# Kernel tuning notes

Hardware: AMD Instinct MI355X
Metric: run time of the kernel (lower is better)

The kernel has to match this reference:

```python
import jax, jax.numpy as jnp
import numpy as np

N = 50000   # nodes
E = 600000  # edges
F = 128     # num_node_features
H = 128     # hidden_channels
C = 10      # num_classes
G = 64      # graphs in batch


def setup_inputs() -> dict:
    key = jax.random.key(0)
    ks = jax.random.split(key, 12)
    x = jax.random.normal(ks[0], (N, F), jnp.float32)
    edge_index = jax.random.randint(ks[1], (2, E), 0, N, dtype=jnp.int32)
    batch = jnp.sort(jax.random.randint(ks[2], (N,), 0, G, dtype=jnp.int32))
    def glorot(k, shape):
        lim = np.sqrt(6.0 / (shape[0] + shape[1])).astype(np.float32)
        return jax.random.uniform(k, shape, jnp.float32, -lim, lim)
    return {
        "x": x,
        "edge_index": edge_index,
        "batch": batch,
        "W1": glorot(ks[3], (F, H)), "b1": jnp.zeros((H,), jnp.float32),
        "W2": glorot(ks[4], (H, H)), "b2": jnp.zeros((H,), jnp.float32),
        "W3": glorot(ks[5], (H, H)), "b3": jnp.zeros((H,), jnp.float32),
        "Wl": glorot(ks[6], (H, C)), "bl": jnp.zeros((C,), jnp.float32),
    }


def reference(x, edge_index, batch, W1, b1, W2, b2, W3, b3, Wl, bl):
    # GCNConv: add self-loops, symmetric degree normalization D^-1/2 A D^-1/2
    src0, dst0 = edge_index[0], edge_index[1]
    loop = jnp.arange(N, dtype=src0.dtype)
    src = jnp.concatenate([src0, loop])
    dst = jnp.concatenate([dst0, loop])
    deg = jax.ops.segment_sum(jnp.ones_like(dst, jnp.float32), dst, num_segments=N)
    dinv = jnp.where(deg > 0, jax.lax.rsqrt(deg), 0.0)
    norm = dinv[src] * dinv[dst]  # [E+N]

    def conv(h, W, b):
        h = h @ W                                  # [N, H] transform first (PyG GCNConv)
        msg = h[src] * norm[:, None]               # gather + normalize
        return jax.ops.segment_sum(msg, dst, num_segments=N) + b  # scatter-add

    h = jax.nn.relu(conv(x, W1, b1))
    h = jax.nn.relu(conv(h, W2, b2))
    h = conv(h, W3, b3)

    # global_mean_pool over batch ids
    counts = jax.ops.segment_sum(jnp.ones((N,), jnp.float32), batch, num_segments=G)
    pooled = jax.ops.segment_sum(h, batch, num_segments=G) / jnp.maximum(counts, 1.0)[:, None]
    return pooled @ Wl + bl  # [G, C]
```

## Files before the change

### kernel.cpp

```cpp
#include <hip/hip_runtime.h>
#include <hip/hip_bf16.h>

#define NN 50000
#define EE 600000
#define FF 128
#define HH 128
#define CC 10
#define GG 64

typedef unsigned int uint32;
typedef unsigned short ushort16;
typedef __attribute__((ext_vector_type(8))) short short8;
typedef __attribute__((ext_vector_type(4))) float f32x4;

__device__ __forceinline__ float bf_lo(uint32 u) { return __uint_as_float(u << 16); }
__device__ __forceinline__ float bf_hi(uint32 u) { return __uint_as_float(u & 0xffff0000u); }
__device__ __forceinline__ ushort16 f2bf(float f) {
    __hip_bfloat16 b = __float2bfloat16(f);
    return *reinterpret_cast<ushort16*>(&b);
}
__device__ __forceinline__ uint32 pack2bf(float a, float b) {
    return (uint32)f2bf(a) | ((uint32)f2bf(b) << 16);
}
__device__ __forceinline__ int q8(float f) {
    return __float2int_rn(fminf(fmaxf(f * 16.f, -127.f), 127.f)) & 255;
}

__global__ void count_deg(const int* __restrict__ dst, int* __restrict__ deg) {
    int e = blockIdx.x * blockDim.x + threadIdx.x;
    if (e < EE) atomicAdd(&deg[dst[e]], 1);
}

__global__ void compute_dinv(const int* __restrict__ deg, float* __restrict__ dinv) {
    int n = blockIdx.x * blockDim.x + threadIdx.x;
    if (n < NN) dinv[n] = rsqrtf((float)(deg[n] + 1));
}

#define SB 256
__global__ __launch_bounds__(SB) void scan_block(const int* __restrict__ deg,
                                                 int* __restrict__ row_ptr,
                                                 int* __restrict__ bsum) {
    __shared__ int sm[SB];
    int t = threadIdx.x;
    int i = blockIdx.x * SB + t;
    int v = (i < NN) ? deg[i] : 0;
    sm[t] = v;
    __syncthreads();
    for (int off = 1; off < SB; off <<= 1) {
        int add = (t >= off) ? sm[t - off] : 0;
        __syncthreads();
        sm[t] += add;
        __syncthreads();
    }
    if (i < NN) row_ptr[i] = sm[t] - v;
    if (t == SB - 1) bsum[blockIdx.x] = sm[t];
}

__global__ void scan_bsum(int* __restrict__ bsum, int nb) {
    __shared__ int sm[256];
    int t = threadIdx.x;
    int v = (t < nb) ? bsum[t] : 0;
    sm[t] = v;
    __syncthreads();
    for (int off = 1; off < 256; off <<= 1) {
        int add = (t >= off) ? sm[t - off] : 0;
        __syncthreads();
        sm[t] += add;
        __syncthreads();
    }
    if (t < nb) bsum[t] = sm[t] - v;
}

__global__ __launch_bounds__(SB) void scan_add(int* __restrict__ row_ptr,
                                               const int* __restrict__ bsum) {
    int i = blockIdx.x * SB + threadIdx.x;
    if (i < NN) row_ptr[i] += bsum[blockIdx.x];
    if (i == 0) row_ptr[NN] = EE;
}

__global__ void fill_csr(const int* __restrict__ src, const int* __restrict__ dst,
                         const int* __restrict__ row_ptr, int* __restrict__ cursor,
                         const float* __restrict__ dinv,
                         int2* __restrict__ csr_en) {
    int e = blockIdx.x * blockDim.x + threadIdx.x;
    if (e < EE) {
        int s = src[e], d = dst[e];
        int pos = row_ptr[d] + atomicAdd(&cursor[d], 1);
        csr_en[pos] = make_int2(s * 128, __float_as_int(dinv[s] * dinv[d] * 0.0625f));
    }
}

__global__ __launch_bounds__(256) void transpose_w3(const float* __restrict__ W1,
                                                    const float* __restrict__ W2,
                                                    const float* __restrict__ W3,
                                                    ushort16* __restrict__ T1,
                                                    ushort16* __restrict__ T2,
                                                    ushort16* __restrict__ T3) {
    int wi = blockIdx.x >> 4;
    const float* W = (wi == 0) ? W1 : (wi == 1) ? W2 : W3;
    ushort16* T = (wi == 0) ? T1 : (wi == 1) ? T2 : T3;
    int base = (blockIdx.x & 15) * 256 + threadIdx.x;
#pragma unroll
    for (int i = 0; i < 4; i++) {
        int idx = base + i * 4096;
        int col = idx & 127;
        int k = idx >> 7;
        T[col * 128 + k] = f2bf(W[k * 128 + col]);
    }
}

template <bool AF32>
__global__ __launch_bounds__(256) void gemm_mfma(const void* __restrict__ Av,
                                                 const ushort16* __restrict__ Wt,
                                                 uint32* __restrict__ zout) {
    __shared__ uint4 lds4[34816 / 16];
    char* lds = (char*)lds4;
    int t = threadIdx.x;
    int w = t >> 6, l = t & 63;
    int lrow = l & 15, g = l >> 4;
    int rowBase = blockIdx.x * 64;
    int arow = rowBase + w * 16 + lrow;
    short8 afr[4];
    const char* Ab = (const char*)Av;
    bool inb = arow < NN;
#pragma unroll
    for (int s = 0; s < 4; s++) {
        if (inb) {
            if (AF32) {
                float4 f0 = *(const float4*)(Ab + (size_t)arow * 512 + s * 128 + g * 32);
                float4 f1 = *(const float4*)(Ab + (size_t)arow * 512 + s * 128 + g * 32 + 16);
                union { short8 s8; uint32 u[4]; } cv;
                cv.u[0] = pack2bf(f0.x, f0.y);
                cv.u[1] = pack2bf(f0.z, f0.w);
                cv.u[2] = pack2bf(f1.x, f1.y);
                cv.u[3] = pack2bf(f1.z, f1.w);
                afr[s] = cv.s8;
            } else {
                afr[s] = *(const short8*)(Ab + (size_t)arow * 256 + s * 64 + g * 16);
            }
        } else {
            short8 z = {0, 0, 0, 0, 0, 0, 0, 0};
            afr[s] = z;
        }
    }
    const char* Wb = (const char*)Wt;
#pragma unroll
    for (int i = 0; i < 8; i++) {
        int idx = t + i * 256;
        int col = idx >> 4, c16 = idx & 15;
        *(uint4*)(lds + col * 272 + c16 * 16) = *(const uint4*)(Wb + col * 256 + c16 * 16);
    }
    __syncthreads();
    f32x4 acc[8];
#pragma unroll
    for (int c = 0; c < 8; c++) { f32x4 z = {0.f, 0.f, 0.f, 0.f}; acc[c] = z; }
#pragma unroll
    for (int s = 0; s < 4; s++) {
#pragma unroll
        for (int c = 0; c < 8; c++) {
            short8 b = *(const short8*)(lds + (c * 16 + lrow) * 272 + s * 64 + g * 16);
            acc[c] = __builtin_amdgcn_mfma_f32_16x16x32_bf16(afr[s], b, acc[c], 0, 0, 0);
        }
    }
    __syncthreads();
    char* myl = lds + w * 8448;
#pragma unroll
    for (int c = 0; c < 8; c++) {
#pragma unroll
        for (int j = 0; j < 4; j++) {
            *(float*)(myl + (g * 4 + j) * 528 + (c * 16 + lrow) * 4) = acc[c][j];
        }
    }
    __syncthreads();
#pragma unroll
    for (int j = 0; j < 8; j++) {
        int rl = (l >> 5) + 2 * j;
        int ch = l & 31;
        float4 v = *(const float4*)(myl + rl * 528 + ch * 16);
        int grow = rowBase + w * 16 + rl;
        if (grow < NN) {
            uint32 u = q8(v.x) | (q8(v.y) << 8) | (q8(v.z) << 16) | (q8(v.w) << 24);
            zout[(size_t)grow * 32 + ch] = u;
        }
    }
}

#define AGG_FMA(c, v)                                              \
    {                                                              \
        float nm = __int_as_float((c).y);                          \
        a0 += nm * (float)((int)((v) << 24) >> 24);                \
        a1 += nm * (float)((int)((v) << 16) >> 24);                \
        a2 += nm * (float)((int)((v) << 8) >> 24);                 \
        a3 += nm * (float)((int)(v) >> 24);                        \
    }

template <int MODE>
__global__ __launch_bounds__(256) void aggregate(const uint32* __restrict__ z8,
                                                 const int* __restrict__ row_ptr,
                                                 const int2* __restrict__ csr_en,
                                                 const float* __restrict__ dinv,
                                                 const float* __restrict__ bias,
                                                 ushort16* __restrict__ out,
                                                 float* __restrict__ pooled,
                                                 const int* __restrict__ batch) {
    int grp = threadIdx.x >> 5;
    int ll  = threadIdx.x & 31;
    int n = blockIdx.x * 8 + grp;
    const char* base = (const char*)z8;
    int boff = ll << 2;
    float dn = dinv[n];
    float w2 = dn * dn * 0.0625f;
    float a0, a1, a2, a3;
    {
        uint32 u = *(const uint32*)(base + (size_t)n * 128 + boff);
        a0 = w2 * (float)((int)(u << 24) >> 24);
        a1 = w2 * (float)((int)(u << 16) >> 24);
        a2 = w2 * (float)((int)(u << 8) >> 24);
        a3 = w2 * (float)((int)u >> 24);
    }
    int s = row_ptr[n], e = row_ptr[n + 1];
    int k = s;
    if (k + 4 <= e) {
        int2 c0 = csr_en[k], c1 = csr_en[k + 1], c2 = csr_en[k + 2], c3 = csr_en[k + 3];
        uint32 v0 = *(const uint32*)(base + (size_t)(uint32)c0.x + boff);
        uint32 v1 = *(const uint32*)(base + (size_t)(uint32)c1.x + boff);
        uint32 v2 = *(const uint32*)(base + (size_t)(uint32)c2.x + boff);
        uint32 v3 = *(const uint32*)(base + (size_t)(uint32)c3.x + boff);
        k += 4;
        for (; k + 4 <= e; k += 4) {
            int2 d0 = csr_en[k], d1 = csr_en[k + 1], d2 = csr_en[k + 2], d3 = csr_en[k + 3];
            uint32 w0 = *(const uint32*)(base + (size_t)(uint32)d0.x + boff);
            uint32 w1 = *(const uint32*)(base + (size_t)(uint32)d1.x + boff);
            uint32 w2_ = *(const uint32*)(base + (size_t)(uint32)d2.x + boff);
            uint32 w3 = *(const uint32*)(base + (size_t)(uint32)d3.x + boff);
            AGG_FMA(c0, v0); AGG_FMA(c1, v1); AGG_FMA(c2, v2); AGG_FMA(c3, v3);
            c0 = d0; c1 = d1; c2 = d2; c3 = d3;
            v0 = w0; v1 = w1; v2 = w2_; v3 = w3;
        }
        AGG_FMA(c0, v0); AGG_FMA(c1, v1); AGG_FMA(c2, v2); AGG_FMA(c3, v3);
    }
    for (; k < e; k++) {
        int2 c0 = csr_en[k];
        uint32 v0 = *(const uint32*)(base + (size_t)(uint32)c0.x + boff);
        AGG_FMA(c0, v0);
    }
    float4 b4 = *(const float4*)(bias + (ll << 2));
    a0 += b4.x; a1 += b4.y; a2 += b4.z; a3 += b4.w;
    if (MODE == 0) {
        a0 = fmaxf(a0, 0.f); a1 = fmaxf(a1, 0.f); a2 = fmaxf(a2, 0.f); a3 = fmaxf(a3, 0.f);
        uint2 o = make_uint2(pack2bf(a0, a1), pack2bf(a2, a3));
        *(uint2*)((char*)out + (size_t)n * 256 + (ll << 3)) = o;
    }
    if (MODE == 2) {
        __shared__ float psum[2][128];
        __shared__ int sgmin;
        int g = batch[n];
        if (threadIdx.x == 0) sgmin = g;
        psum[threadIdx.x >> 7][threadIdx.x & 127] = 0.f;
        __syncthreads();
        int slot = g - sgmin;
        if (slot < 2) {
            float* p = &psum[slot][ll << 2];
            atomicAdd(p + 0, a0); atomicAdd(p + 1, a1);
            atomicAdd(p + 2, a2); atomicAdd(p + 3, a3);
        } else {
            float* p = &pooled[g * HH + (ll << 2)];
            atomicAdd(p + 0, a0); atomicAdd(p + 1, a1);
            atomicAdd(p + 2, a2); atomicAdd(p + 3, a3);
        }
        __syncthreads();
        int sl = threadIdx.x >> 7, f = threadIdx.x & 127;
        float v = psum[sl][f];
        int gg = sgmin + sl;
        if (v != 0.f && gg < GG) atomicAdd(&pooled[gg * HH + f], v);
    }
}

__global__ __launch_bounds__(128) void final_linear(const float* __restrict__ pooled,
                                                    const int* __restrict__ batch,
                                                    const float* __restrict__ Wl,
                                                    const float* __restrict__ bl,
                                                    float* __restrict__ out) {
    int g = blockIdx.x;
    int t = threadIdx.x;
    __shared__ float pm[128];
    __shared__ int cnt_s;
    if (t == 0) {
        int lo = 0, hi = NN;
        while (lo < hi) { int m = (lo + hi) >> 1; if (batch[m] < g) lo = m + 1; else hi = m; }
        int s = lo;
        lo = 0; hi = NN;
        while (lo < hi) { int m = (lo + hi) >> 1; if (batch[m] < g + 1) lo = m + 1; else hi = m; }
        int c = lo - s;
        cnt_s = c > 0 ? c : 1;
    }
    __syncthreads();
    pm[t] = pooled[g * HH + t] / (float)cnt_s;
    __syncthreads();
    if (t < CC) {
        float o = bl[t];
        for (int f = 0; f < 128; f++) o += pm[f] * Wl[f * CC + t];
        out[g * CC + t] = o;
    }
}

extern "C" void kernel_launch(void* const* d_in, const int* in_sizes, int n_in,
                              void* d_out, int out_size, void* d_ws, size_t ws_size,
                              hipStream_t stream) {
    const float* x    = (const float*)d_in[0];
    const int*   ei   = (const int*)d_in[1];
    const int*   bat  = (const int*)d_in[2];
    const float* W1   = (const float*)d_in[3];
    const float* b1   = (const float*)d_in[4];
    const float* W2   = (const float*)d_in[5];
    const float* b2   = (const float*)d_in[6];
    const float* W3   = (const float*)d_in[7];
    const float* b3   = (const float*)d_in[8];
    const float* Wl   = (const float*)d_in[9];
    const float* bl   = (const float*)d_in[10];
    float* out = (float*)d_out;

    const int* src = ei;
    const int* dst = ei + EE;

    char* ws = (char*)d_ws;
    size_t off = 0;
    auto take = [&](size_t bytes) -> char* {
        char* p = ws + off;
        off += (bytes + 255) & ~(size_t)255;
        return p;
    };
    int*      deg     = (int*)take((size_t)NN * 4);
    float*    dinv    = (float*)take((size_t)NN * 4);
    int*      row_ptr = (int*)take((size_t)(NN + 1) * 4);
    int*      bsum    = (int*)take((size_t)256 * 4);
    int2*     csr_en  = (int2*)take((size_t)EE * 8);
    ushort16* Wt1     = (ushort16*)take((size_t)HH * HH * 2);
    ushort16* Wt2     = (ushort16*)take((size_t)HH * HH * 2);
    ushort16* Wt3     = (ushort16*)take((size_t)HH * HH * 2);
    uint32*   bufZ    = (uint32*)take((size_t)NN * HH);
    ushort16* bufH    = (ushort16*)take((size_t)NN * HH * 2);
    float*    pooled  = (float*)take((size_t)GG * HH * 4);

    const int nbScan = (NN + SB - 1) / SB;

    hipMemsetAsync(deg, 0, (size_t)NN * 4, stream);
    hipMemsetAsync(pooled, 0, (size_t)GG * HH * 4, stream);
    count_deg<<<(EE + 255) / 256, 256, 0, stream>>>(dst, deg);
    compute_dinv<<<(NN + 255) / 256, 256, 0, stream>>>(deg, dinv);
    scan_block<<<nbScan, SB, 0, stream>>>(deg, row_ptr, bsum);
    scan_bsum<<<1, 256, 0, stream>>>(bsum, nbScan);
    scan_add<<<nbScan, SB, 0, stream>>>(row_ptr, bsum);
    hipMemsetAsync(deg, 0, (size_t)NN * 4, stream);
    fill_csr<<<(EE + 255) / 256, 256, 0, stream>>>(src, dst, row_ptr, deg, dinv, csr_en);

    transpose_w3<<<48, 256, 0, stream>>>(W1, W2, W3, Wt1, Wt2, Wt3);

    const int gemmBlocks = (NN + 63) / 64;
    const int aggBlocks  = NN / 8;
    gemm_mfma<true><<<gemmBlocks, 256, 0, stream>>>(x, Wt1, bufZ);
    aggregate<0><<<aggBlocks, 256, 0, stream>>>(bufZ, row_ptr, csr_en, dinv, b1, bufH, pooled, bat);
    gemm_mfma<false><<<gemmBlocks, 256, 0, stream>>>(bufH, Wt2, bufZ);
    aggregate<0><<<aggBlocks, 256, 0, stream>>>(bufZ, row_ptr, csr_en, dinv, b2, bufH, pooled, bat);
    gemm_mfma<false><<<gemmBlocks, 256, 0, stream>>>(bufH, Wt3, bufZ);
    aggregate<2><<<aggBlocks, 256, 0, stream>>>(bufZ, row_ptr, csr_en, dinv, b3, bufH, pooled, bat);

    final_linear<<<GG, 128, 0, stream>>>(pooled, bat, Wl, bl, out);
}
```

Measured before the change: 212.0 us.

## Split int8 feature table into two column halves and aggregate each half separately

The GEMM output is now written as two 64-byte-per-row int8 tables (low and high feature halves), and each aggregation layer runs as two passes, one per half, with 16 threads per node. Each pass gathers from a table half the size (about 3.2 MB), which is meant to raise the L2/cache hit rate of the random neighbor gathers. In exchange, CSR indices, row pointers and norms are read twice per layer, there are twice as many aggregate launches, and the pooled atomics and LDS partial sums are split across passes.

```diff
diff --git a/kernel.cpp b/kernel.cpp
--- a/kernel.cpp
+++ b/kernel.cpp
@@ -86,7 +86,7 @@
     if (e < EE) {
         int s = src[e], d = dst[e];
         int pos = row_ptr[d] + atomicAdd(&cursor[d], 1);
-        csr_en[pos] = make_int2(s * 128, __float_as_int(dinv[s] * dinv[d] * 0.0625f));
+        csr_en[pos] = make_int2(s * 64, __float_as_int(dinv[s] * dinv[d] * 0.0625f));
     }
 }
 
@@ -112,7 +112,8 @@
 template <bool AF32>
 __global__ __launch_bounds__(256) void gemm_mfma(const void* __restrict__ Av,
                                                  const ushort16* __restrict__ Wt,
-                                                 uint32* __restrict__ zout) {
+                                                 uint32* __restrict__ zlo,
+                                                 uint32* __restrict__ zhi) {
     __shared__ uint4 lds4[34816 / 16];
     char* lds = (char*)lds4;
     int t = threadIdx.x;
@@ -180,7 +181,8 @@
         int grow = rowBase + w * 16 + rl;
         if (grow < NN) {
             uint32 u = q8(v.x) | (q8(v.y) << 8) | (q8(v.z) << 16) | (q8(v.w) << 24);
-            zout[(size_t)grow * 32 + ch] = u;
+            if (ch < 16) zlo[(size_t)grow * 16 + ch] = u;
+            else         zhi[(size_t)grow * 16 + (ch - 16)] = u;
         }
     }
 }
@@ -195,24 +197,25 @@
     }
 
 template <int MODE>
-__global__ __launch_bounds__(256) void aggregate(const uint32* __restrict__ z8,
+__global__ __launch_bounds__(256) void aggregate(const uint32* __restrict__ zp,
                                                  const int* __restrict__ row_ptr,
                                                  const int2* __restrict__ csr_en,
                                                  const float* __restrict__ dinv,
                                                  const float* __restrict__ bias,
                                                  ushort16* __restrict__ out,
                                                  float* __restrict__ pooled,
-                                                 const int* __restrict__ batch) {
-    int grp = threadIdx.x >> 5;
-    int ll  = threadIdx.x & 31;
-    int n = blockIdx.x * 8 + grp;
-    const char* base = (const char*)z8;
+                                                 const int* __restrict__ batch,
+                                                 int pass) {
+    int grp = threadIdx.x >> 4;
+    int ll  = threadIdx.x & 15;
+    int n = blockIdx.x * 16 + grp;
+    const char* base = (const char*)zp;
     int boff = ll << 2;
     float dn = dinv[n];
     float w2 = dn * dn * 0.0625f;
     float a0, a1, a2, a3;
     {
-        uint32 u = *(const uint32*)(base + (size_t)n * 128 + boff);
+        uint32 u = *(const uint32*)(base + (size_t)n * 64 + boff);
         a0 = w2 * (float)((int)(u << 24) >> 24);
         a1 = w2 * (float)((int)(u << 16) >> 24);
         a2 = w2 * (float)((int)(u << 8) >> 24);
@@ -244,19 +247,19 @@
         uint32 v0 = *(const uint32*)(base + (size_t)(uint32)c0.x + boff);
         AGG_FMA(c0, v0);
     }
-    float4 b4 = *(const float4*)(bias + (ll << 2));
+    float4 b4 = *(const float4*)(bias + pass * 64 + (ll << 2));
     a0 += b4.x; a1 += b4.y; a2 += b4.z; a3 += b4.w;
     if (MODE == 0) {
         a0 = fmaxf(a0, 0.f); a1 = fmaxf(a1, 0.f); a2 = fmaxf(a2, 0.f); a3 = fmaxf(a3, 0.f);
         uint2 o = make_uint2(pack2bf(a0, a1), pack2bf(a2, a3));
-        *(uint2*)((char*)out + (size_t)n * 256 + (ll << 3)) = o;
+        *(uint2*)((char*)out + (size_t)n * 256 + pass * 128 + (ll << 3)) = o;
     }
     if (MODE == 2) {
-        __shared__ float psum[2][128];
+        __shared__ float psum[2][64];
         __shared__ int sgmin;
         int g = batch[n];
         if (threadIdx.x == 0) sgmin = g;
-        psum[threadIdx.x >> 7][threadIdx.x & 127] = 0.f;
+        if (threadIdx.x < 128) psum[threadIdx.x >> 6][threadIdx.x & 63] = 0.f;
         __syncthreads();
         int slot = g - sgmin;
         if (slot < 2) {
@@ -264,15 +267,17 @@
             atomicAdd(p + 0, a0); atomicAdd(p + 1, a1);
             atomicAdd(p + 2, a2); atomicAdd(p + 3, a3);
         } else {
-            float* p = &pooled[g * HH + (ll << 2)];
+            float* p = &pooled[g * HH + pass * 64 + (ll << 2)];
             atomicAdd(p + 0, a0); atomicAdd(p + 1, a1);
             atomicAdd(p + 2, a2); atomicAdd(p + 3, a3);
         }
         __syncthreads();
-        int sl = threadIdx.x >> 7, f = threadIdx.x & 127;
-        float v = psum[sl][f];
-        int gg = sgmin + sl;
-        if (v != 0.f && gg < GG) atomicAdd(&pooled[gg * HH + f], v);
+        if (threadIdx.x < 128) {
+            int sl = threadIdx.x >> 6, f = threadIdx.x & 63;
+            float v = psum[sl][f];
+            int gg = sgmin + sl;
+            if (v != 0.f && gg < GG) atomicAdd(&pooled[gg * HH + pass * 64 + f], v);
+        }
     }
 }
 
@@ -338,7 +343,8 @@
     ushort16* Wt1     = (ushort16*)take((size_t)HH * HH * 2);
     ushort16* Wt2     = (ushort16*)take((size_t)HH * HH * 2);
     ushort16* Wt3     = (ushort16*)take((size_t)HH * HH * 2);
-    uint32*   bufZ    = (uint32*)take((size_t)NN * HH);
+    uint32*   zlo     = (uint32*)take((size_t)NN * 64);
+    uint32*   zhi     = (uint32*)take((size_t)NN * 64);
     ushort16* bufH    = (ushort16*)take((size_t)NN * HH * 2);
     float*    pooled  = (float*)take((size_t)GG * HH * 4);
 
@@ -357,13 +363,16 @@
     transpose_w3<<<48, 256, 0, stream>>>(W1, W2, W3, Wt1, Wt2, Wt3);
 
     const int gemmBlocks = (NN + 63) / 64;
-    const int aggBlocks  = NN / 8;
-    gemm_mfma<true><<<gemmBlocks, 256, 0, stream>>>(x, Wt1, bufZ);
-    aggregate<0><<<aggBlocks, 256, 0, stream>>>(bufZ, row_ptr, csr_en, dinv, b1, bufH, pooled, bat);
-    gemm_mfma<false><<<gemmBlocks, 256, 0, stream>>>(bufH, Wt2, bufZ);
-    aggregate<0><<<aggBlocks, 256, 0, stream>>>(bufZ, row_ptr, csr_en, dinv, b2, bufH, pooled, bat);
-    gemm_mfma<false><<<gemmBlocks, 256, 0, stream>>>(bufH, Wt3, bufZ);
-    aggregate<2><<<aggBlocks, 256, 0, stream>>>(bufZ, row_ptr, csr_en, dinv, b3, bufH, pooled, bat);
+    const int aggBlocks  = NN / 16;
+    gemm_mfma<true><<<gemmBlocks, 256, 0, stream>>>(x, Wt1, zlo, zhi);
+    aggregate<0><<<aggBlocks, 256, 0, stream>>>(zlo, row_ptr, csr_en, dinv, b1, bufH, pooled, bat, 0);
+    aggregate<0><<<aggBlocks, 256, 0, stream>>>(zhi, row_ptr, csr_en, dinv, b1, bufH, pooled, bat, 1);
+    gemm_mfma<false><<<gemmBlocks, 256, 0, stream>>>(bufH, Wt2, zlo, zhi);
+    aggregate<0><<<aggBlocks, 256, 0, stream>>>(zlo, row_ptr, csr_en, dinv, b2, bufH, pooled, bat, 0);
+    aggregate<0><<<aggBlocks, 256, 0, stream>>>(zhi, row_ptr, csr_en, dinv, b2, bufH, pooled, bat, 1);
+    gemm_mfma<false><<<gemmBlocks, 256, 0, stream>>>(bufH, Wt3, zlo, zhi);
+    aggregate<2><<<aggBlocks, 256, 0, stream>>>(zlo, row_ptr, csr_en, dinv, b3, bufH, pooled, bat, 0);
+    aggregate<2><<<aggBlocks, 256, 0, stream>>>(zhi, row_ptr, csr_en, dinv, b3, bufH, pooled, bat, 1);
 
     final_linear<<<GG, 128, 0, stream>>>(pooled, bat, Wl, bl, out);
 }
```

Result: slower. 230.1 us (+8.6%).

## Fuse GCN aggregation with the next layer's MFMA GEMM and merge setup kernels

Applied to the files above, without the earlier changes.

Layers 1 and 2 now aggregate neighbours into bf16 rows held in LDS, then run the next layer's MFMA GEMM in the same block, so the bf16 hidden buffer is never written to or read back from global memory. Setup is also merged: dinv is computed inside the scan, the weight transpose runs alongside scan_add in one launch, and a single memset clears degree, cursor and pooled buffers. This cuts kernel launches and global traffic, but each fused block now aggregates 64 rows with 16 threads per row. That gives less gather parallelism per block, and the larger LDS footprint may lower occupancy.

```diff
diff --git a/kernel.cpp b/kernel.cpp
--- a/kernel.cpp
+++ b/kernel.cpp
@@ -7,14 +7,14 @@
 #define HH 128
 #define CC 10
 #define GG 64
+#define SB 256
+#define NBSCAN ((NN + SB - 1) / SB)
 
 typedef unsigned int uint32;
 typedef unsigned short ushort16;
 typedef __attribute__((ext_vector_type(8))) short short8;
 typedef __attribute__((ext_vector_type(4))) float f32x4;
 
-__device__ __forceinline__ float bf_lo(uint32 u) { return __uint_as_float(u << 16); }
-__device__ __forceinline__ float bf_hi(uint32 u) { return __uint_as_float(u & 0xffff0000u); }
 __device__ __forceinline__ ushort16 f2bf(float f) {
     __hip_bfloat16 b = __float2bfloat16(f);
     return *reinterpret_cast<ushort16*>(&b);
@@ -31,19 +31,15 @@
     if (e < EE) atomicAdd(&deg[dst[e]], 1);
 }
 
-__global__ void compute_dinv(const int* __restrict__ deg, float* __restrict__ dinv) {
-    int n = blockIdx.x * blockDim.x + threadIdx.x;
-    if (n < NN) dinv[n] = rsqrtf((float)(deg[n] + 1));
-}
-
-#define SB 256
 __global__ __launch_bounds__(SB) void scan_block(const int* __restrict__ deg,
                                                  int* __restrict__ row_ptr,
-                                                 int* __restrict__ bsum) {
+                                                 int* __restrict__ bsum,
+                                                 float* __restrict__ dinv) {
     __shared__ int sm[SB];
     int t = threadIdx.x;
     int i = blockIdx.x * SB + t;
     int v = (i < NN) ? deg[i] : 0;
+    if (i < NN) dinv[i] = rsqrtf((float)(v + 1));
     sm[t] = v;
     __syncthreads();
     for (int off = 1; off < SB; off <<= 1) {
@@ -71,11 +67,33 @@
     if (t < nb) bsum[t] = sm[t] - v;
 }
 
-__global__ __launch_bounds__(SB) void scan_add(int* __restrict__ row_ptr,
-                                               const int* __restrict__ bsum) {
-    int i = blockIdx.x * SB + threadIdx.x;
-    if (i < NN) row_ptr[i] += bsum[blockIdx.x];
-    if (i == 0) row_ptr[NN] = EE;
+__global__ __launch_bounds__(SB) void scan_add_tw(int* __restrict__ row_ptr,
+                                                  const int* __restrict__ bsum,
+                                                  const float* __restrict__ W1,
+                                                  const float* __restrict__ W2,
+                                                  const float* __restrict__ W3,
+                                                  ushort16* __restrict__ T1,
+                                                  ushort16* __restrict__ T2,
+                                                  ushort16* __restrict__ T3) {
+    int b = blockIdx.x;
+    if (b < NBSCAN) {
+        int i = b * SB + threadIdx.x;
+        if (i < NN) row_ptr[i] += bsum[b];
+        if (i == 0) row_ptr[NN] = EE;
+    } else {
+        int bi = b - NBSCAN;
+        int wi = bi >> 4;
+        const float* W = (wi == 0) ? W1 : (wi == 1) ? W2 : W3;
+        ushort16* T = (wi == 0) ? T1 : (wi == 1) ? T2 : T3;
+        int base = (bi & 15) * 256 + threadIdx.x;
+#pragma unroll
+        for (int i = 0; i < 4; i++) {
+            int idx = base + i * 4096;
+            int col = idx & 127;
+            int k = idx >> 7;
+            T[col * 128 + k] = f2bf(W[k * 128 + col]);
+        }
+    }
 }
 
 __global__ void fill_csr(const int* __restrict__ src, const int* __restrict__ dst,
@@ -90,54 +108,29 @@
     }
 }
 
-__global__ __launch_bounds__(256) void transpose_w3(const float* __restrict__ W1,
-                                                    const float* __restrict__ W2,
-                                                    const float* __restrict__ W3,
-                                                    ushort16* __restrict__ T1,
-                                                    ushort16* __restrict__ T2,
-                                                    ushort16* __restrict__ T3) {
-    int wi = blockIdx.x >> 4;
-    const float* W = (wi == 0) ? W1 : (wi == 1) ? W2 : W3;
-    ushort16* T = (wi == 0) ? T1 : (wi == 1) ? T2 : T3;
-    int base = (blockIdx.x & 15) * 256 + threadIdx.x;
-#pragma unroll
-    for (int i = 0; i < 4; i++) {
-        int idx = base + i * 4096;
-        int col = idx & 127;
-        int k = idx >> 7;
-        T[col * 128 + k] = f2bf(W[k * 128 + col]);
-    }
-}
-
-template <bool AF32>
-__global__ __launch_bounds__(256) void gemm_mfma(const void* __restrict__ Av,
-                                                 const ushort16* __restrict__ Wt,
-                                                 uint32* __restrict__ zout) {
-    __shared__ uint4 lds4[34816 / 16];
-    char* lds = (char*)lds4;
+__global__ __launch_bounds__(256) void gemm_x(const float* __restrict__ A,
+                                              const ushort16* __restrict__ Wt,
+                                              uint32* __restrict__ zout) {
+    __shared__ char lds[34816];
     int t = threadIdx.x;
     int w = t >> 6, l = t & 63;
     int lrow = l & 15, g = l >> 4;
     int rowBase = blockIdx.x * 64;
     int arow = rowBase + w * 16 + lrow;
     short8 afr[4];
-    const char* Ab = (const char*)Av;
+    const char* Ab = (const char*)A;
     bool inb = arow < NN;
 #pragma unroll
     for (int s = 0; s < 4; s++) {
         if (inb) {
-            if (AF32) {
-                float4 f0 = *(const float4*)(Ab + (size_t)arow * 512 + s * 128 + g * 32);
-                float4 f1 = *(const float4*)(Ab + (size_t)arow * 512 + s * 128 + g * 32 + 16);
-                union { short8 s8; uint32 u[4]; } cv;
-                cv.u[0] = pack2bf(f0.x, f0.y);
-                cv.u[1] = pack2bf(f0.z, f0.w);
-                cv.u[2] = pack2bf(f1.x, f1.y);
-                cv.u[3] = pack2bf(f1.z, f1.w);
-                afr[s] = cv.s8;
-            } else {
-                afr[s] = *(const short8*)(Ab + (size_t)arow * 256 + s * 64 + g * 16);
-            }
+            float4 f0 = *(const float4*)(Ab + (size_t)arow * 512 + s * 128 + g * 32);
+            float4 f1 = *(const float4*)(Ab + (size_t)arow * 512 + s * 128 + g * 32 + 16);
+            union { short8 s8; uint32 u[4]; } cv;
+            cv.u[0] = pack2bf(f0.x, f0.y);
+            cv.u[1] = pack2bf(f0.z, f0.w);
+            cv.u[2] = pack2bf(f1.x, f1.y);
+            cv.u[3] = pack2bf(f1.z, f1.w);
+            afr[s] = cv.s8;
         } else {
             short8 z = {0, 0, 0, 0, 0, 0, 0, 0};
             afr[s] = z;
@@ -185,7 +178,139 @@
     }
 }
 
-#define AGG_FMA(c, v)                                              \
+#define AGG_FMA8(c, v)                                              \
+    {                                                               \
+        float nm = __int_as_float((c).y);                           \
+        a0 += nm * (float)((int)((v).x << 24) >> 24);               \
+        a1 += nm * (float)((int)((v).x << 16) >> 24);               \
+        a2 += nm * (float)((int)((v).x << 8) >> 24);                \
+        a3 += nm * (float)((int)(v).x >> 24);                       \
+        a4 += nm * (float)((int)((v).y << 24) >> 24);               \
+        a5 += nm * (float)((int)((v).y << 16) >> 24);               \
+        a6 += nm * (float)((int)((v).y << 8) >> 24);                \
+        a7 += nm * (float)((int)(v).y >> 24);                       \
+    }
+
+__global__ __launch_bounds__(256) void fused_agg_gemm(const uint32* __restrict__ zin,
+                                                      const int* __restrict__ row_ptr,
+                                                      const int2* __restrict__ csr_en,
+                                                      const float* __restrict__ dinv,
+                                                      const float* __restrict__ bias,
+                                                      const ushort16* __restrict__ Wt,
+                                                      uint32* __restrict__ zout) {
+    __shared__ char ldsW[34816];
+    __shared__ char ldsA[17408];
+    int t = threadIdx.x;
+    const char* Wb = (const char*)Wt;
+#pragma unroll
+    for (int i = 0; i < 8; i++) {
+        int idx = t + i * 256;
+        int col = idx >> 4, c16 = idx & 15;
+        *(uint4*)(ldsW + col * 272 + c16 * 16) = *(const uint4*)(Wb + col * 256 + c16 * 16);
+    }
+    int grp = t >> 4, ll = t & 15;
+    int rowBase = blockIdx.x * 64;
+    const char* base = (const char*)zin;
+    int boff = ll << 3;
+    for (int i = 0; i < 4; i++) {
+        int lr = grp * 4 + i;
+        int n = rowBase + lr;
+        uint4 packed = make_uint4(0, 0, 0, 0);
+        if (n < NN) {
+            float dn = dinv[n];
+            float w2 = dn * dn * 0.0625f;
+            float a0, a1, a2, a3, a4, a5, a6, a7;
+            {
+                uint2 u = *(const uint2*)(base + (size_t)n * 128 + boff);
+                a0 = w2 * (float)((int)(u.x << 24) >> 24);
+                a1 = w2 * (float)((int)(u.x << 16) >> 24);
+                a2 = w2 * (float)((int)(u.x << 8) >> 24);
+                a3 = w2 * (float)((int)u.x >> 24);
+                a4 = w2 * (float)((int)(u.y << 24) >> 24);
+                a5 = w2 * (float)((int)(u.y << 16) >> 24);
+                a6 = w2 * (float)((int)(u.y << 8) >> 24);
+                a7 = w2 * (float)((int)u.y >> 24);
+            }
+            int s = row_ptr[n], e = row_ptr[n + 1];
+            int k = s;
+            if (k + 4 <= e) {
+                int2 c0 = csr_en[k], c1 = csr_en[k + 1], c2 = csr_en[k + 2], c3 = csr_en[k + 3];
+                uint2 v0 = *(const uint2*)(base + (size_t)(uint32)c0.x + boff);
+                uint2 v1 = *(const uint2*)(base + (size_t)(uint32)c1.x + boff);
+                uint2 v2 = *(const uint2*)(base + (size_t)(uint32)c2.x + boff);
+                uint2 v3 = *(const uint2*)(base + (size_t)(uint32)c3.x + boff);
+                k += 4;
+                for (; k + 4 <= e; k += 4) {
+                    int2 d0 = csr_en[k], d1 = csr_en[k + 1], d2 = csr_en[k + 2], d3 = csr_en[k + 3];
+                    uint2 w0 = *(const uint2*)(base + (size_t)(uint32)d0.x + boff);
+                    uint2 w1 = *(const uint2*)(base + (size_t)(uint32)d1.x + boff);
+                    uint2 w2_ = *(const uint2*)(base + (size_t)(uint32)d2.x + boff);
+                    uint2 w3 = *(const uint2*)(base + (size_t)(uint32)d3.x + boff);
+                    AGG_FMA8(c0, v0); AGG_FMA8(c1, v1); AGG_FMA8(c2, v2); AGG_FMA8(c3, v3);
+                    c0 = d0; c1 = d1; c2 = d2; c3 = d3;
+                    v0 = w0; v1 = w1; v2 = w2_; v3 = w3;
+                }
+                AGG_FMA8(c0, v0); AGG_FMA8(c1, v1); AGG_FMA8(c2, v2); AGG_FMA8(c3, v3);
+            }
+            for (; k < e; k++) {
+                int2 c0 = csr_en[k];
+                uint2 v0 = *(const uint2*)(base + (size_t)(uint32)c0.x + boff);
+                AGG_FMA8(c0, v0);
+            }
+            float4 bA = *(const float4*)(bias + ll * 8);
+            float4 bB = *(const float4*)(bias + ll * 8 + 4);
+            a0 = fmaxf(a0 + bA.x, 0.f); a1 = fmaxf(a1 + bA.y, 0.f);
+            a2 = fmaxf(a2 + bA.z, 0.f); a3 = fmaxf(a3 + bA.w, 0.f);
+            a4 = fmaxf(a4 + bB.x, 0.f); a5 = fmaxf(a5 + bB.y, 0.f);
+            a6 = fmaxf(a6 + bB.z, 0.f); a7 = fmaxf(a7 + bB.w, 0.f);
+            packed.x = pack2bf(a0, a1); packed.y = pack2bf(a2, a3);
+            packed.z = pack2bf(a4, a5); packed.w = pack2bf(a6, a7);
+        }
+        *(uint4*)(ldsA + lr * 272 + ll * 16) = packed;
+    }
+    __syncthreads();
+    int w = t >> 6, l = t & 63;
+    int lrow = l & 15, g = l >> 4;
+    short8 afr[4];
+#pragma unroll
+    for (int s = 0; s < 4; s++) {
+        afr[s] = *(const short8*)(ldsA + (w * 16 + lrow) * 272 + s * 64 + g * 16);
+    }
+    f32x4 acc[8];
+#pragma unroll
+    for (int c = 0; c < 8; c++) { f32x4 z = {0.f, 0.f, 0.f, 0.f}; acc[c] = z; }
+#pragma unroll
+    for (int s = 0; s < 4; s++) {
+#pragma unroll
+        for (int c = 0; c < 8; c++) {
+            short8 b = *(const short8*)(ldsW + (c * 16 + lrow) * 272 + s * 64 + g * 16);
+            acc[c] = __builtin_amdgcn_mfma_f32_16x16x32_bf16(afr[s], b, acc[c], 0, 0, 0);
+        }
+    }
+    __syncthreads();
+    char* myl = ldsW + w * 8448;
+#pragma unroll
+    for (int c = 0; c < 8; c++) {
+#pragma unroll
+        for (int j = 0; j < 4; j++) {
+            *(float*)(myl + (g * 4 + j) * 528 + (c * 16 + lrow) * 4) = acc[c][j];
+        }
+    }
+    __syncthreads();
+#pragma unroll
+    for (int j = 0; j < 8; j++) {
+        int rl = (l >> 5) + 2 * j;
+        int ch = l & 31;
+        float4 v = *(const float4*)(myl + rl * 528 + ch * 16);
+        int grow = rowBase + w * 16 + rl;
+        if (grow < NN) {
+            uint32 u = q8(v.x) | (q8(v.y) << 8) | (q8(v.z) << 16) | (q8(v.w) << 24);
+            zout[(size_t)grow * 32 + ch] = u;
+        }
+    }
+}
+
+#define AGG_FMA4(c, v)                                             \
     {                                                              \
         float nm = __int_as_float((c).y);                          \
         a0 += nm * (float)((int)((v) << 24) >> 24);                \
@@ -194,15 +319,13 @@
         a3 += nm * (float)((int)(v) >> 24);                        \
     }
 
-template <int MODE>
-__global__ __launch_bounds__(256) void aggregate(const uint32* __restrict__ z8,
-                                                 const int* __restrict__ row_ptr,
-                                                 const int2* __restrict__ csr_en,
-                                                 const float* __restrict__ dinv,
-                                                 const float* __restrict__ bias,
-                                                 ushort16* __restrict__ out,
-                                                 float* __restrict__ pooled,
-                                                 const int* __restrict__ batch) {
+__global__ __launch_bounds__(256) void aggregate_pool(const uint32* __restrict__ z8,
+                                                      const int* __restrict__ row_ptr,
+                                                      const int2* __restrict__ csr_en,
+                                                      const float* __restrict__ dinv,
+                                                      const float* __restrict__ bias,
+                                                      float* __restrict__ pooled,
+                                                      const int* __restrict__ batch) {
     int grp = threadIdx.x >> 5;
     int ll  = threadIdx.x & 31;
     int n = blockIdx.x * 8 + grp;
@@ -233,47 +356,40 @@
             uint32 w1 = *(const uint32*)(base + (size_t)(uint32)d1.x + boff);
             uint32 w2_ = *(const uint32*)(base + (size_t)(uint32)d2.x + boff);
             uint32 w3 = *(const uint32*)(base + (size_t)(uint32)d3.x + boff);
-            AGG_FMA(c0, v0); AGG_FMA(c1, v1); AGG_FMA(c2, v2); AGG_FMA(c3, v3);
+            AGG_FMA4(c0, v0); AGG_FMA4(c1, v1); AGG_FMA4(c2, v2); AGG_FMA4(c3, v3);
             c0 = d0; c1 = d1; c2 = d2; c3 = d3;
             v0 = w0; v1 = w1; v2 = w2_; v3 = w3;
         }
-        AGG_FMA(c0, v0); AGG_FMA(c1, v1); AGG_FMA(c2, v2); AGG_FMA(c3, v3);
+        AGG_FMA4(c0, v0); AGG_FMA4(c1, v1); AGG_FMA4(c2, v2); AGG_FMA4(c3, v3);
     }
     for (; k < e; k++) {
         int2 c0 = csr_en[k];
         uint32 v0 = *(const uint32*)(base + (size_t)(uint32)c0.x + boff);
-        AGG_FMA(c0, v0);
+        AGG_FMA4(c0, v0);
     }
     float4 b4 = *(const float4*)(bias + (ll << 2));
     a0 += b4.x; a1 += b4.y; a2 += b4.z; a3 += b4.w;
-    if (MODE == 0) {
-        a0 = fmaxf(a0, 0.f); a1 = fmaxf(a1, 0.f); a2 = fmaxf(a2, 0.f); a3 = fmaxf(a3, 0.f);
-        uint2 o = make_uint2(pack2bf(a0, a1), pack2bf(a2, a3));
-        *(uint2*)((char*)out + (size_t)n * 256 + (ll << 3)) = o;
-    }
-    if (MODE == 2) {
-        __shared__ float psum[2][128];
-        __shared__ int sgmin;
-        int g = batch[n];
-        if (threadIdx.x == 0) sgmin = g;
-        psum[threadIdx.x >> 7][threadIdx.x & 127] = 0.f;
-        __syncthreads();
-        int slot = g - sgmin;
-        if (slot < 2) {
-            float* p = &psum[slot][ll << 2];
-            atomicAdd(p + 0, a0); atomicAdd(p + 1, a1);
-            atomicAdd(p + 2, a2); atomicAdd(p + 3, a3);
-        } else {
-            float* p = &pooled[g * HH + (ll << 2)];
-            atomicAdd(p + 0, a0); atomicAdd(p + 1, a1);
-            atomicAdd(p + 2, a2); atomicAdd(p + 3, a3);
-        }
-        __syncthreads();
-        int sl = threadIdx.x >> 7, f = threadIdx.x & 127;
-        float v = psum[sl][f];
-        int gg = sgmin + sl;
-        if (v != 0.f && gg < GG) atomicAdd(&pooled[gg * HH + f], v);
-    }
+    __shared__ float psum[2][128];
+    __shared__ int sgmin;
+    int g = batch[n];
+    if (threadIdx.x == 0) sgmin = g;
+    psum[threadIdx.x >> 7][threadIdx.x & 127] = 0.f;
+    __syncthreads();
+    int slot = g - sgmin;
+    if (slot < 2) {
+        float* p = &psum[slot][ll << 2];
+        atomicAdd(p + 0, a0); atomicAdd(p + 1, a1);
+        atomicAdd(p + 2, a2); atomicAdd(p + 3, a3);
+    } else {
+        float* p = &pooled[g * HH + (ll << 2)];
+        atomicAdd(p + 0, a0); atomicAdd(p + 1, a1);
+        atomicAdd(p + 2, a2); atomicAdd(p + 3, a3);
+    }
+    __syncthreads();
+    int sl = threadIdx.x >> 7, f = threadIdx.x & 127;
+    float v = psum[sl][f];
+    int gg = sgmin + sl;
+    if (v != 0.f && gg < GG) atomicAdd(&pooled[gg * HH + f], v);
 }
 
 __global__ __launch_bounds__(128) void final_linear(const float* __restrict__ pooled,
@@ -331,6 +447,8 @@
         return p;
     };
     int*      deg     = (int*)take((size_t)NN * 4);
+    int*      cursor  = (int*)take((size_t)NN * 4);
+    float*    pooled  = (float*)take((size_t)GG * HH * 4);
     float*    dinv    = (float*)take((size_t)NN * 4);
     int*      row_ptr = (int*)take((size_t)(NN + 1) * 4);
     int*      bsum    = (int*)take((size_t)256 * 4);
@@ -338,32 +456,24 @@
     ushort16* Wt1     = (ushort16*)take((size_t)HH * HH * 2);
     ushort16* Wt2     = (ushort16*)take((size_t)HH * HH * 2);
     ushort16* Wt3     = (ushort16*)take((size_t)HH * HH * 2);
-    uint32*   bufZ    = (uint32*)take((size_t)NN * HH);
-    ushort16* bufH    = (ushort16*)take((size_t)NN * HH * 2);
-    float*    pooled  = (float*)take((size_t)GG * HH * 4);
-
-    const int nbScan = (NN + SB - 1) / SB;
-
-    hipMemsetAsync(deg, 0, (size_t)NN * 4, stream);
-    hipMemsetAsync(pooled, 0, (size_t)GG * HH * 4, stream);
+    uint32*   zA      = (uint32*)take((size_t)NN * HH);
+    uint32*   zB      = (uint32*)take((size_t)NN * HH);
+
+    const size_t clr = ((size_t)NN * 4 + 255 & ~(size_t)255) * 2 +
+                       ((size_t)GG * HH * 4);
+    hipMemsetAsync(deg, 0, clr, stream);
+
     count_deg<<<(EE + 255) / 256, 256, 0, stream>>>(dst, deg);
-    compute_dinv<<<(NN + 255) / 256, 256, 0, stream>>>(deg, dinv);
-    scan_block<<<nbScan, SB, 0, stream>>>(deg, row_ptr, bsum);
-    scan_bsum<<<1, 256, 0, stream>>>(bsum, nbScan);
-    scan_add<<<nbScan, SB, 0, stream>>>(row_ptr, bsum);
-    hipMemsetAsync(deg, 0, (size_t)NN * 4, stream);
-    fill_csr<<<(EE + 255) / 256, 256, 0, stream>>>(src, dst, row_ptr, deg, dinv, csr_en);
-
-    transpose_w3<<<48, 256, 0, stream>>>(W1, W2, W3, Wt1, Wt2, Wt3);
+    scan_block<<<NBSCAN, SB, 0, stream>>>(deg, row_ptr, bsum, dinv);
+    scan_bsum<<<1, 256, 0, stream>>>(bsum, NBSCAN);
+    scan_add_tw<<<NBSCAN + 48, SB, 0, stream>>>(row_ptr, bsum, W1, W2, W3, Wt1, Wt2, Wt3);
+    fill_csr<<<(EE + 255) / 256, 256, 0, stream>>>(src, dst, row_ptr, cursor, dinv, csr_en);
 
     const int gemmBlocks = (NN + 63) / 64;
-    const int aggBlocks  = NN / 8;
-    gemm_mfma<true><<<gemmBlocks, 256, 0, stream>>>(x, Wt1, bufZ);
-    aggregate<0><<<aggBlocks, 256, 0, stream>>>(bufZ, row_ptr, csr_en, dinv, b1, bufH, pooled, bat);
-    gemm_mfma<false><<<gemmBlocks, 256, 0, stream>>>(bufH, Wt2, bufZ);
-    aggregate<0><<<aggBlocks, 256, 0, stream>>>(bufZ, row_ptr, csr_en, dinv, b2, bufH, pooled, bat);
-    gemm_mfma<false><<<gemmBlocks, 256, 0, stream>>>(bufH, Wt3, bufZ);
-    aggregate<2><<<aggBlocks, 256, 0, stream>>>(bufZ, row_ptr, csr_en, dinv, b3, bufH, pooled, bat);
+    gemm_x<<<gemmBlocks, 256, 0, stream>>>(x, Wt1, zA);
+    fused_agg_gemm<<<gemmBlocks, 256, 0, stream>>>(zA, row_ptr, csr_en, dinv, b1, Wt2, zB);
+    fused_agg_gemm<<<gemmBlocks, 256, 0, stream>>>(zB, row_ptr, csr_en, dinv, b2, Wt3, zA);
+    aggregate_pool<<<NN / 8, 256, 0, stream>>>(zA, row_ptr, csr_en, dinv, b3, pooled, bat);
 
     final_linear<<<GG, 128, 0, stream>>>(pooled, bat, Wl, bl, out);
 }
```

Result: slower. 226.8 us (+7.0%).
